# Kernel optimization log

Hardware: AMD Instinct MI355X
Metric: run time of the kernel (lower is better)

The kernel has to match this reference:

```python
import jax, jax.numpy as jnp
import numpy as np

B, S, E, H = 4, 8192, 1024, 16
D = E // H  # head_dim = 64


def setup_inputs() -> dict:
    key = jax.random.key(0)
    ks = jax.random.split(key, 9)
    s = 0.02
    return {
        "x": jax.random.normal(ks[0], (B, S, E), dtype=jnp.float32),
        "Wq": jax.random.normal(ks[1], (D, E), dtype=jnp.float32) * s,
        "bq": jax.random.normal(ks[2], (D,), dtype=jnp.float32) * s,
        "Wk": jax.random.normal(ks[3], (D, E), dtype=jnp.float32) * s,
        "bk": jax.random.normal(ks[4], (D,), dtype=jnp.float32) * s,
        "Wv": jax.random.normal(ks[5], (D, E), dtype=jnp.float32) * s,
        "bv": jax.random.normal(ks[6], (D,), dtype=jnp.float32) * s,
        "Wo": jax.random.normal(ks[7], (E, E), dtype=jnp.float32) * s,
        "bo": jax.random.normal(ks[8], (E,), dtype=jnp.float32) * s,
    }


def reference(x, Wq, bq, Wk, bk, Wv, bv, Wo, bo):
    b, s, e = x.shape
    d = Wq.shape[0]          # head_dim (projections map embed_dim -> head_dim)
    h = e // d               # num_heads
    # torch Linear: y = x @ W.T + b ; projected shape [B, S, d]
    # view(B, -1, h, d) on [B, S, d] => effective seq S' = S // h (faithful to source)
    def split_heads(t):
        return t.reshape(b, -1, h, d).transpose(0, 2, 1, 3)  # [B, H, S', D]
    q = split_heads(x @ Wq.T + bq)
    k = split_heads(x @ Wk.T + bk)
    v = split_heads(x @ Wv.T + bv)
    scores = jnp.einsum('bhqd,bhkd->bhqk', q, k) / np.sqrt(d).astype(jnp.float32)
    attn = jax.nn.softmax(scores, axis=-1)  # dropout=0.0 => identity
    ctx = jnp.einsum('bhqk,bhkd->bhqd', attn, v)
    ctx = ctx.transpose(0, 2, 1, 3).reshape(b, -1, e)  # [B, S', E]
    return ctx @ Wo.T + bo
```

## Files before the change

kernel.cpp:

```cpp
#include <hip/hip_runtime.h>
#include <hip/hip_bf16.h>


typedef unsigned short u16;
typedef __attribute__((ext_vector_type(8))) short short8;
typedef __attribute__((ext_vector_type(4))) float f32x4;

__device__ inline u16 f2bf(float f) {
    union { float f; unsigned u; } v; v.f = f;
    unsigned u = v.u;
    return (u16)((u + 0x7fffu + ((u >> 16) & 1u)) >> 16);
}
__device__ inline unsigned pack_bf2(float a, float b) {
    union { __hip_bfloat162 h; unsigned u; } v;
    v.h = __float22bfloat162_rn(float2{a, b});
    return v.u;
}
__device__ __forceinline__ void gld16(void* lds, const void* gptr) {
    __builtin_amdgcn_global_load_lds(
        (const __attribute__((address_space(1))) unsigned int*)gptr,
        (__attribute__((address_space(3))) unsigned int*)lds,
        16, 0, 0);
}

__global__ __launch_bounds__(256) void convw(
    const float* __restrict__ Wq, const float* __restrict__ bq,
    const float* __restrict__ Wk, const float* __restrict__ bk,
    const float* __restrict__ Wv, const float* __restrict__ bv,
    const float* __restrict__ Wo,
    u16* __restrict__ Wqkv, float* __restrict__ qkvb, u16* __restrict__ Wob)
{
    const int idx = blockIdx.x * 256 + threadIdx.x;
    Wob[idx] = f2bf(Wo[idx]);
    if (idx < 196608) {
        const int row = idx >> 10, k = idx & 1023;
        float v = (row < 64)  ? Wq[row * 1024 + k] * 0.125f
                : (row < 128) ? Wk[(row - 64) * 1024 + k]
                              : Wv[(row - 128) * 1024 + k];
        Wqkv[idx] = f2bf(v);
    }
    if (idx < 192) {
        qkvb[idx] = (idx < 64) ? bq[idx] * 0.125f
                  : (idx < 128) ? bk[idx - 64] : bv[idx - 128];
    }
}

__global__ __launch_bounds__(256) void qkv_gemm(
    const float* __restrict__ X, const u16* __restrict__ W,
    const float* __restrict__ bias, u16* __restrict__ Out)
{
    __shared__ short8 Bs[2][1536];

    const int tid = threadIdx.x;
    const int lane = tid & 63, wid = tid >> 6;
    const int q = lane >> 4, r = lane & 15;
    const long m0 = (long)blockIdx.x * 64;

    const u16* wp[6];
    #pragma unroll
    for (int i = 0; i < 6; ++i) {
        const int p = wid * 6 + i, kk2 = p / 12, nt = p % 12;
        wp[i] = W + (long)(nt * 16 + r) * 1024 + kk2 * 32 + q * 8;
    }

    const float* px = X + (m0 + wid * 16 + r) * 1024 + q * 8;

    f32x4 acc[12] = {};

    #pragma unroll
    for (int i = 0; i < 6; ++i)
        gld16(&Bs[0][(wid * 6 + i) * 64], wp[i]);
    float4 a[4];
    a[0] = *(const float4*)(px);
    a[1] = *(const float4*)(px + 4);
    a[2] = *(const float4*)(px + 32);
    a[3] = *(const float4*)(px + 36);
    __syncthreads();

    for (int k0 = 0; k0 < 1024; k0 += 64) {
        const int buf = (k0 >> 6) & 1;
        float4 an[4] = {};
        if (k0 + 64 < 1024) {
            #pragma unroll
            for (int i = 0; i < 6; ++i)
                gld16(&Bs[buf ^ 1][(wid * 6 + i) * 64], wp[i] + k0 + 64);
            an[0] = *(const float4*)(px + k0 + 64);
            an[1] = *(const float4*)(px + k0 + 68);
            an[2] = *(const float4*)(px + k0 + 96);
            an[3] = *(const float4*)(px + k0 + 100);
        }
        #pragma unroll
        for (int kk2 = 0; kk2 < 2; ++kk2) {
            union { short8 s; unsigned u[4]; } af;
            af.u[0] = pack_bf2(a[kk2 * 2].x, a[kk2 * 2].y);
            af.u[1] = pack_bf2(a[kk2 * 2].z, a[kk2 * 2].w);
            af.u[2] = pack_bf2(a[kk2 * 2 + 1].x, a[kk2 * 2 + 1].y);
            af.u[3] = pack_bf2(a[kk2 * 2 + 1].z, a[kk2 * 2 + 1].w);
            #pragma unroll
            for (int nt = 0; nt < 12; ++nt)
                acc[nt] = __builtin_amdgcn_mfma_f32_16x16x32_bf16(
                    af.s, Bs[buf][(kk2 * 12 + nt) * 64 + lane], acc[nt], 0, 0, 0);
        }
        __syncthreads();
        #pragma unroll
        for (int i = 0; i < 4; ++i) a[i] = an[i];
    }

    #pragma unroll
    for (int nt = 0; nt < 12; ++nt) {
        const int col = nt * 16 + r;
        const float badd = bias[col];
        #pragma unroll
        for (int e = 0; e < 4; ++e) {
            const long row = m0 + wid * 16 + q * 4 + e;
            Out[row * 192 + col] = f2bf(acc[nt][e] + badd);
        }
    }
}

__global__ __launch_bounds__(256) void vtrans(
    const u16* __restrict__ qkv, u16* __restrict__ Vt)
{
    __shared__ u16 T[64][68];
    const int bh = blockIdx.x, b = bh >> 4, h = bh & 15;
    const int i0 = blockIdx.y * 64;
    const int tid = threadIdx.x;

    #pragma unroll
    for (int it = 0; it < 2; ++it) {
        const int c = tid + 256 * it;
        const int il = c >> 3, d8 = (c & 7) * 8;
        short8 v = *(const short8*)(qkv +
            ((long)b * 8192 + (long)(i0 + il) * 16 + h) * 192 + 128 + d8);
        #pragma unroll
        for (int j = 0; j < 8; ++j) T[d8 + j][il] = (u16)v[j];
    }
    __syncthreads();
    #pragma unroll
    for (int it = 0; it < 2; ++it) {
        const int c = tid + 256 * it;
        const int dl = c >> 3, i8 = (c & 7) * 8;
        short8 o;
        #pragma unroll
        for (int j = 0; j < 8; ++j) o[j] = (short)T[dl][i8 + j];
        *(short8*)(Vt + ((long)bh * 64 + dl) * 512 + i0 + i8) = o;
    }
}

__global__ __launch_bounds__(256) void attn_flash(
    const u16* __restrict__ qkv, const u16* __restrict__ Vt,
    u16* __restrict__ ctx)
{
    __shared__ short8 Ks[2][512];
    __shared__ short8 Vs[2][512];
    __shared__ u16 Plds[4][16 * 72];

    const int tid = threadIdx.x, lane = tid & 63, wid = tid >> 6;
    const int q = lane >> 4, r = lane & 15;
    const int qt = blockIdx.x;
    const int bh = blockIdx.y;
    const int b = bh >> 4, h = bh & 15;
    const long qrowbase = (long)b * 8192 + h;

    short8 Qf0, Qf1;
    {
        const int i = qt * 64 + wid * 16 + r;
        const u16* p = qkv + (qrowbase + (long)i * 16) * 192 + q * 8;
        Qf0 = *(const short8*)(p);
        Qf1 = *(const short8*)(p + 32);
    }

    const u16* kbase = qkv + (qrowbase + (long)(wid * 16 + r) * 16) * 192
                           + 64 + q * 8;
    const u16* vbase = Vt + ((long)bh * 64 + wid * 16 + r) * 512 + q * 8;

    gld16(&Ks[0][wid * 64],       kbase);
    gld16(&Ks[0][256 + wid * 64], kbase + 32);
    gld16(&Vs[0][wid * 64],       vbase);
    gld16(&Vs[0][256 + wid * 64], vbase + 32);
    __syncthreads();

    f32x4 O[4] = {};
    float mrun = -1e30f, lrun = 0.f;
    u16* Pw = &Plds[wid][0];

    for (int c = 0; c < 8; ++c) {
        const int j0 = c * 64, buf = c & 1;
        if (c < 7) {
            const u16* kp = kbase + (long)(j0 + 64) * 3072;
            const u16* vp = vbase + j0 + 64;
            gld16(&Ks[buf ^ 1][wid * 64],       kp);
            gld16(&Ks[buf ^ 1][256 + wid * 64], kp + 32);
            gld16(&Vs[buf ^ 1][wid * 64],       vp);
            gld16(&Vs[buf ^ 1][256 + wid * 64], vp + 32);
        }
        f32x4 S[4];
        #pragma unroll
        for (int ct = 0; ct < 4; ++ct) {
            f32x4 s = {};
            s = __builtin_amdgcn_mfma_f32_16x16x32_bf16(
                Ks[buf][ct * 64 + lane], Qf0, s, 0, 0, 0);
            s = __builtin_amdgcn_mfma_f32_16x16x32_bf16(
                Ks[buf][256 + ct * 64 + lane], Qf1, s, 0, 0, 0);
            S[ct] = s;
        }
        float mc = -1e30f;
        #pragma unroll
        for (int ct = 0; ct < 4; ++ct)
            mc = fmaxf(mc, fmaxf(fmaxf(S[ct][0], S[ct][1]),
                                 fmaxf(S[ct][2], S[ct][3])));
        mc = fmaxf(mc, __shfl_xor(mc, 16, 64));
        mc = fmaxf(mc, __shfl_xor(mc, 32, 64));
        const float mnew = fmaxf(mrun, mc);
        const float alpha = __expf(mrun - mnew);
        mrun = mnew;
        float se = 0.f;
        #pragma unroll
        for (int ct = 0; ct < 4; ++ct)
            #pragma unroll
            for (int e = 0; e < 4; ++e) {
                const float pv = __expf(S[ct][e] - mnew);
                S[ct][e] = pv; se += pv;
            }
        se += __shfl_xor(se, 16, 64);
        se += __shfl_xor(se, 32, 64);
        lrun = lrun * alpha + se;
        #pragma unroll
        for (int nt = 0; nt < 4; ++nt)
            #pragma unroll
            for (int e = 0; e < 4; ++e) O[nt][e] *= alpha;
        #pragma unroll
        for (int ct = 0; ct < 4; ++ct) {
            uint2 d;
            d.x = pack_bf2(S[ct][0], S[ct][1]);
            d.y = pack_bf2(S[ct][2], S[ct][3]);
            *(uint2*)(Pw + r * 72 + ct * 16 + q * 4) = d;
        }
        short8 Pf0 = *(const short8*)(Pw + r * 72 + q * 8);
        short8 Pf1 = *(const short8*)(Pw + r * 72 + 32 + q * 8);
        #pragma unroll
        for (int nt = 0; nt < 4; ++nt) {
            O[nt] = __builtin_amdgcn_mfma_f32_16x16x32_bf16(
                Vs[buf][nt * 64 + lane], Pf0, O[nt], 0, 0, 0);
            O[nt] = __builtin_amdgcn_mfma_f32_16x16x32_bf16(
                Vs[buf][256 + nt * 64 + lane], Pf1, O[nt], 0, 0, 0);
        }
        __syncthreads();
    }

    const float inv = 1.0f / lrun;
    const long i = qt * 64 + wid * 16 + r;
    u16* po = ctx + ((long)b * 512 + i) * 1024 + h * 64;
    #pragma unroll
    for (int nt = 0; nt < 4; ++nt) {
        uint2 d;
        d.x = pack_bf2(O[nt][0] * inv, O[nt][1] * inv);
        d.y = pack_bf2(O[nt][2] * inv, O[nt][3] * inv);
        *(uint2*)(po + nt * 16 + q * 4) = d;
    }
}

__global__ __launch_bounds__(256) void gemm_o(
    const u16* __restrict__ A, const u16* __restrict__ B,
    const float* __restrict__ bias, float* __restrict__ C)
{
    __shared__ short8 As[2][512];
    __shared__ short8 Bs[2][512];

    const int tid = threadIdx.x;
    const int lane = tid & 63, wid = tid >> 6;
    const int q = lane >> 4, r = lane & 15;
    const long m0 = (long)blockIdx.x * 64, n0 = (long)blockIdx.y * 64;
    const int wm = wid >> 1, wn = wid & 1;

    const u16* ap[2];
    const u16* bp[2];
    #pragma unroll
    for (int i = 0; i < 2; ++i) {
        const int t = wid * 2 + i, f = t >> 2, mt = t & 3;
        ap[i] = A + (m0 + mt * 16 + r) * 1024 + f * 32 + q * 8;
        bp[i] = B + (n0 + mt * 16 + r) * 1024 + f * 32 + q * 8;
    }

    #pragma unroll
    for (int i = 0; i < 2; ++i) {
        gld16(&As[0][(wid * 2 + i) * 64], ap[i]);
        gld16(&Bs[0][(wid * 2 + i) * 64], bp[i]);
    }
    __syncthreads();

    f32x4 acc[2][2] = {};

    for (int k0 = 0; k0 < 1024; k0 += 64) {
        const int buf = (k0 >> 6) & 1;
        if (k0 + 64 < 1024) {
            #pragma unroll
            for (int i = 0; i < 2; ++i) {
                gld16(&As[buf ^ 1][(wid * 2 + i) * 64], ap[i] + k0 + 64);
                gld16(&Bs[buf ^ 1][(wid * 2 + i) * 64], bp[i] + k0 + 64);
            }
        }
        #pragma unroll
        for (int f = 0; f < 2; ++f) {
            short8 af0 = As[buf][f * 256 + (wm * 2 + 0) * 64 + lane];
            short8 af1 = As[buf][f * 256 + (wm * 2 + 1) * 64 + lane];
            short8 bf0 = Bs[buf][f * 256 + (wn * 2 + 0) * 64 + lane];
            short8 bf1 = Bs[buf][f * 256 + (wn * 2 + 1) * 64 + lane];
            acc[0][0] = __builtin_amdgcn_mfma_f32_16x16x32_bf16(af0, bf0, acc[0][0], 0, 0, 0);
            acc[0][1] = __builtin_amdgcn_mfma_f32_16x16x32_bf16(af0, bf1, acc[0][1], 0, 0, 0);
            acc[1][0] = __builtin_amdgcn_mfma_f32_16x16x32_bf16(af1, bf0, acc[1][0], 0, 0, 0);
            acc[1][1] = __builtin_amdgcn_mfma_f32_16x16x32_bf16(af1, bf1, acc[1][1], 0, 0, 0);
        }
        __syncthreads();
    }

    #pragma unroll
    for (int i = 0; i < 2; ++i)
        #pragma unroll
        for (int j = 0; j < 2; ++j) {
            const long col = n0 + (wn * 2 + j) * 16 + r;
            const float badd = bias[col];
            #pragma unroll
            for (int e = 0; e < 4; ++e) {
                const long row = m0 + (wm * 2 + i) * 16 + q * 4 + e;
                C[row * 1024 + col] = acc[i][j][e] + badd;
            }
        }
}

extern "C" void kernel_launch(void* const* d_in, const int* in_sizes, int n_in,
                              void* d_out, int out_size, void* d_ws, size_t ws_size,
                              hipStream_t stream)
{
    const float* x  = (const float*)d_in[0];
    const float* Wq = (const float*)d_in[1];
    const float* bq = (const float*)d_in[2];
    const float* Wk = (const float*)d_in[3];
    const float* bk = (const float*)d_in[4];
    const float* Wv = (const float*)d_in[5];
    const float* bv = (const float*)d_in[6];
    const float* Wo = (const float*)d_in[7];
    const float* bo = (const float*)d_in[8];
    float* out = (float*)d_out;
    char* ws = (char*)d_ws;

    u16*   qkv  = (u16*)(ws);
    u16*   Vt   = (u16*)(ws + 12582912);
    u16*   Wqkv = (u16*)(ws + 16777216);
    u16*   Wob  = (u16*)(ws + 17170432);
    float* qkvb = (float*)(ws + 19267584);
    u16*   ctx  = (u16*)(ws + 19268352);

    convw<<<4096, 256, 0, stream>>>(Wq, bq, Wk, bk, Wv, bv, Wo, Wqkv, qkvb, Wob);
    qkv_gemm<<<512, 256, 0, stream>>>(x, Wqkv, qkvb, qkv);
    vtrans<<<dim3(64, 8), 256, 0, stream>>>(qkv, Vt);
    attn_flash<<<dim3(8, 64), 256, 0, stream>>>(qkv, Vt, ctx);
    gemm_o<<<dim3(32, 16), 256, 0, stream>>>(ctx, Wob, bo, out);
}
```

Before: 263.0 us.

## Use partial vmcnt waits for real double-buffer overlap and stage QKV output through LDS

Replaces __syncthreads in the three pipelined loops with explicit s_waitcnt vmcnt(N) plus raw barriers. The current tile's loads can then be waited on while the next tile's prefetch stays in flight, where a full drain previously stalled every iteration. The QKV projection epilogue also stages its bf16 results through the freed LDS buffer and writes them out as coalesced 16-byte stores instead of scattered 2-byte stores. The hand-counted vmcnt values depend on exact load ordering, and a wrong count would cause a race.

```diff
diff --git a/kernel.cpp b/kernel.cpp
--- a/kernel.cpp
+++ b/kernel.cpp
@@ -5,6 +5,10 @@
 typedef unsigned short u16;
 typedef __attribute__((ext_vector_type(8))) short short8;
 typedef __attribute__((ext_vector_type(4))) float f32x4;
+
+#define VMWAIT(N) asm volatile("s_waitcnt vmcnt(" #N ")" ::: "memory")
+#define MEMFENCE() asm volatile("" ::: "memory")
+#define BAR() __builtin_amdgcn_s_barrier()
 
 __device__ inline u16 f2bf(float f) {
     union { float f; unsigned u; } v; v.f = f;
@@ -75,7 +79,6 @@
     a[1] = *(const float4*)(px + 4);
     a[2] = *(const float4*)(px + 32);
     a[3] = *(const float4*)(px + 36);
-    __syncthreads();
 
     for (int k0 = 0; k0 < 1024; k0 += 64) {
         const int buf = (k0 >> 6) & 1;
@@ -88,7 +91,12 @@
             an[1] = *(const float4*)(px + k0 + 68);
             an[2] = *(const float4*)(px + k0 + 96);
             an[3] = *(const float4*)(px + k0 + 100);
-        }
+            VMWAIT(10);
+        } else {
+            VMWAIT(0);
+        }
+        BAR();
+        MEMFENCE();
         #pragma unroll
         for (int kk2 = 0; kk2 < 2; ++kk2) {
             union { short8 s; unsigned u[4]; } af;
@@ -101,20 +109,26 @@
                 acc[nt] = __builtin_amdgcn_mfma_f32_16x16x32_bf16(
                     af.s, Bs[buf][(kk2 * 12 + nt) * 64 + lane], acc[nt], 0, 0, 0);
         }
-        __syncthreads();
+        MEMFENCE();
+        BAR();
         #pragma unroll
         for (int i = 0; i < 4; ++i) a[i] = an[i];
     }
 
+    u16* reg = (u16*)(&Bs[0][0]) + wid * 3072;
     #pragma unroll
     for (int nt = 0; nt < 12; ++nt) {
-        const int col = nt * 16 + r;
-        const float badd = bias[col];
-        #pragma unroll
-        for (int e = 0; e < 4; ++e) {
-            const long row = m0 + wid * 16 + q * 4 + e;
-            Out[row * 192 + col] = f2bf(acc[nt][e] + badd);
-        }
+        const float badd = bias[nt * 16 + r];
+        #pragma unroll
+        for (int e = 0; e < 4; ++e)
+            reg[(q * 4 + e) * 192 + nt * 16 + r] = f2bf(acc[nt][e] + badd);
+    }
+    asm volatile("s_waitcnt lgkmcnt(0)" ::: "memory");
+    u16* ob = Out + (m0 + wid * 16) * 192;
+    #pragma unroll
+    for (int t = 0; t < 6; ++t) {
+        short8 v = *(const short8*)(reg + t * 512 + lane * 8);
+        *(short8*)(ob + t * 512 + lane * 8) = v;
     }
 }
 
@@ -178,7 +192,6 @@
     gld16(&Ks[0][256 + wid * 64], kbase + 32);
     gld16(&Vs[0][wid * 64],       vbase);
     gld16(&Vs[0][256 + wid * 64], vbase + 32);
-    __syncthreads();
 
     f32x4 O[4] = {};
     float mrun = -1e30f, lrun = 0.f;
@@ -193,7 +206,12 @@
             gld16(&Ks[buf ^ 1][256 + wid * 64], kp + 32);
             gld16(&Vs[buf ^ 1][wid * 64],       vp);
             gld16(&Vs[buf ^ 1][256 + wid * 64], vp + 32);
-        }
+            VMWAIT(4);
+        } else {
+            VMWAIT(0);
+        }
+        BAR();
+        MEMFENCE();
         f32x4 S[4];
         #pragma unroll
         for (int ct = 0; ct < 4; ++ct) {
@@ -245,7 +263,8 @@
             O[nt] = __builtin_amdgcn_mfma_f32_16x16x32_bf16(
                 Vs[buf][256 + nt * 64 + lane], Pf1, O[nt], 0, 0, 0);
         }
-        __syncthreads();
+        MEMFENCE();
+        BAR();
     }
 
     const float inv = 1.0f / lrun;
@@ -287,7 +306,6 @@
         gld16(&As[0][(wid * 2 + i) * 64], ap[i]);
         gld16(&Bs[0][(wid * 2 + i) * 64], bp[i]);
     }
-    __syncthreads();
 
     f32x4 acc[2][2] = {};
 
@@ -299,7 +317,12 @@
                 gld16(&As[buf ^ 1][(wid * 2 + i) * 64], ap[i] + k0 + 64);
                 gld16(&Bs[buf ^ 1][(wid * 2 + i) * 64], bp[i] + k0 + 64);
             }
-        }
+            VMWAIT(4);
+        } else {
+            VMWAIT(0);
+        }
+        BAR();
+        MEMFENCE();
         #pragma unroll
         for (int f = 0; f < 2; ++f) {
             short8 af0 = As[buf][f * 256 + (wm * 2 + 0) * 64 + lane];
@@ -311,7 +334,8 @@
             acc[1][0] = __builtin_amdgcn_mfma_f32_16x16x32_bf16(af1, bf0, acc[1][0], 0, 0, 0);
             acc[1][1] = __builtin_amdgcn_mfma_f32_16x16x32_bf16(af1, bf1, acc[1][1], 0, 0, 0);
         }
-        __syncthreads();
+        MEMFENCE();
+        BAR();
     }
 
     #pragma unroll
```

After: 261.2 us. Within noise of the previous version (-0.7%).
